# Performance work log

Hardware: AMD Instinct MI355X
Metric: run time of the kernel (lower is better)

Reference implementation:

```python
import jax, jax.numpy as jnp
import numpy as np

D_POINTS = 256
D_MODEL = 512
B, N = 8, 2048


def setup_inputs() -> dict:
    key = jax.random.key(0)
    ks = jax.random.split(key, 6)
    s_in = 1.0 / np.sqrt(D_POINTS)
    s_mid = 1.0 / np.sqrt(D_MODEL)
    return {
        "features": jax.random.normal(ks[0], (B, N, D_POINTS), dtype=jnp.float32),
        "Wq": jax.random.uniform(ks[1], (D_POINTS, D_MODEL), jnp.float32, -s_in, s_in),
        "Wk": jax.random.uniform(ks[2], (D_POINTS, D_MODEL), jnp.float32, -s_in, s_in),
        "Wv": jax.random.uniform(ks[3], (D_POINTS, D_MODEL), jnp.float32, -s_in, s_in),
        "W2": jax.random.uniform(ks[4], (D_MODEL, D_POINTS), jnp.float32, -s_mid, s_mid),
        "b2": jax.random.uniform(ks[5], (D_POINTS,), jnp.float32, -s_mid, s_mid),
    }


def reference(features, Wq, Wk, Wv, W2, b2):
    # features: [B, N, d_points]
    q = jnp.einsum("bnd,dm->bnm", features, Wq)  # [B, N, d_model]
    k = jnp.einsum("bnd,dm->bnm", features, Wk)
    v = jnp.einsum("bnd,dm->bnm", features, Wv)
    scale = 1.0 / np.sqrt(k.shape[-1]).astype(np.float32)
    attn = jax.nn.softmax(jnp.einsum("bnm,bkm->bnk", q, k) * scale, axis=-1)  # [B, N, N]
    res = jnp.einsum("bnk,bkm->bnm", attn, v)  # [B, N, d_model]
    res = jnp.einsum("bnm,md->bnd", res, W2) + b2  # fc2 -> [B, N, d_points]
    res = jax.nn.leaky_relu(res, negative_slope=0.2)
    return res + features
```

## Files before the change

### kernel.cpp

```cpp
#include <hip/hip_runtime.h>
#include <cstdint>

#define NBATCH 8
#define NSEQ   2048
#define NROWS  16384

typedef __attribute__((ext_vector_type(4))) float  f32x4;
typedef __attribute__((ext_vector_type(8))) short  short8;
typedef __attribute__((ext_vector_type(8))) __bf16 bf16x8;
typedef __attribute__((ext_vector_type(8))) _Float16 h8;

#define XB_OFF   0ul
#define WALL_OFF 8388608ul
#define Q_OFF    9175040ul
#define K_OFF    25952256ul
#define VT_OFF   42729472ul
#define W2T_OFF  59506688ul
#define S_OFF    59768832ul

#define SCALE_Q 0.063758746f

__device__ __forceinline__ unsigned short f2bf(float f) {
  unsigned u = __builtin_bit_cast(unsigned, f);
  return (unsigned short)((u + 0x7fffu + ((u >> 16) & 1u)) >> 16);
}

__device__ __forceinline__ f32x4 mfma16(short8 a, short8 b, f32x4 c) {
  return __builtin_amdgcn_mfma_f32_16x16x32_bf16(
      __builtin_bit_cast(bf16x8, a), __builtin_bit_cast(bf16x8, b), c, 0, 0, 0);
}

__device__ __forceinline__ void glds16(const void* g, void* l) {
  __builtin_amdgcn_global_load_lds(
      (const __attribute__((address_space(1))) void*)g,
      (__attribute__((address_space(3))) void*)l, 16, 0, 0);
}

#define BAR_LGKM()                                           \
  {                                                          \
    asm volatile("s_waitcnt lgkmcnt(0)" ::: "memory");       \
    __builtin_amdgcn_sched_barrier(0);                       \
    __builtin_amdgcn_s_barrier();                            \
    __builtin_amdgcn_sched_barrier(0);                       \
  }
#define BAR_ALL()                                                    \
  {                                                                  \
    asm volatile("s_waitcnt vmcnt(0) lgkmcnt(0)" ::: "memory");      \
    __builtin_amdgcn_sched_barrier(0);                               \
    __builtin_amdgcn_s_barrier();                                    \
    __builtin_amdgcn_sched_barrier(0);                               \
  }

__global__ __launch_bounds__(256, 4) void prep_kernel(
    const float* __restrict__ feat, const float* __restrict__ Wq,
    const float* __restrict__ Wk, const float* __restrict__ Wv,
    const float* __restrict__ W2, char* __restrict__ ws) {
  int tid = blockIdx.x * 256 + threadIdx.x;
  if (tid < 524288) {
    int r = tid >> 5, co = (tid & 31) * 8;
    const float* src = feat + (size_t)r * 256 + co;
    short8 v;
#pragma unroll
    for (int i = 0; i < 8; ++i) v[i] = (short)f2bf(src[i]);
    unsigned short* Xb = (unsigned short*)(ws + XB_OFF);
    *(short8*)(Xb + (size_t)r * 256 + (co ^ ((r & 7) << 3))) = v;
  } else if (tid < 917504) {
    int t2 = tid - 524288;
    int m = t2 >> 8, d = t2 & 255;
    int wsel = m >> 9, mm = m & 511;
    const float* W = (wsel == 0) ? Wq : ((wsel == 1) ? Wk : Wv);
    float v = W[(size_t)d * 512 + mm];
    if (wsel == 0) v *= SCALE_Q;
    unsigned short* Wall = (unsigned short*)(ws + WALL_OFF);
    Wall[(size_t)m * 256 + (d ^ ((m & 7) << 3))] = f2bf(v);
  } else {
    int t3 = tid - 917504;
    int d = t3 >> 9, c = t3 & 511;
    unsigned short* W2t = (unsigned short*)(ws + W2T_OFF);
    W2t[(size_t)d * 512 + c] = f2bf(W2[(size_t)c * 256 + d]);
  }
}

__global__ __launch_bounds__(256, 2) void proj_kernel(char* __restrict__ ws) {
  __shared__ char smem[65536];
  const int tid = threadIdx.x;
  const int l = tid & 63, w = tid >> 6;
  const int g = l >> 4, m16 = l & 15;
  const int orig = blockIdx.x;
  const int wgid = (orig & 7) * 192 + (orig >> 3);
  const int nt = wgid % 12, mtb = wgid / 12;
  const char* XbT = ws + XB_OFF + (size_t)mtb * 65536;
  const char* WallT = ws + WALL_OFF + (size_t)nt * 65536;

  auto stage = [&](int buf, int kt) {
#pragma unroll
    for (int j = 0; j < 4; ++j) {
      int idx = j * 256 + tid;
      int r = idx >> 3, p = idx & 7;
      glds16(XbT + r * 512 + kt * 128 + p * 16, smem + buf * 16384 + idx * 16);
      glds16(WallT + r * 512 + kt * 128 + p * 16,
             smem + 32768 + buf * 16384 + idx * 16);
    }
  };

  const int mr = (w >> 1) * 64, nr = (w & 1) * 64;
  const int fxor = (m16 & 7) << 4;
  const f32x4 fz = {0.f, 0.f, 0.f, 0.f};
  f32x4 acc[4][4];
#pragma unroll
  for (int i = 0; i < 4; ++i)
#pragma unroll
    for (int j = 0; j < 4; ++j) acc[i][j] = fz;

  stage(0, 0);
  BAR_ALL();
#pragma unroll 1
  for (int kt = 0; kt < 4; ++kt) {
    if (kt < 3) stage((kt + 1) & 1, kt + 1);
    const char* Ab = smem + (kt & 1) * 16384;
    const char* Bb = smem + 32768 + (kt & 1) * 16384;
#pragma unroll
    for (int ks = 0; ks < 2; ++ks) {
      int off = (16 * g + 64 * ks) ^ fxor;
      short8 af[4], bf[4];
#pragma unroll
      for (int i = 0; i < 4; ++i)
        af[i] = *(const short8*)(Ab + (mr + i * 16 + m16) * 128 + off);
#pragma unroll
      for (int i = 0; i < 4; ++i)
        bf[i] = *(const short8*)(Bb + (nr + i * 16 + m16) * 128 + off);
#pragma unroll
      for (int mi = 0; mi < 4; ++mi)
#pragma unroll
        for (int ni = 0; ni < 4; ++ni)
          acc[mi][ni] = mfma16(af[mi], bf[ni], acc[mi][ni]);
    }
    BAR_ALL();
  }

  const int colg = nt * 128 + nr;
  const int tcat = colg >> 9;
  const int cin_base = colg & 511;
  char* wbuf = smem + w * 2048;
  if (tcat < 2) {
    char* dst = ws + (tcat == 0 ? Q_OFF : K_OFF) +
                ((size_t)(mtb * 8 + (cin_base >> 6))) * 16384;
#pragma unroll
    for (int mi = 0; mi < 4; ++mi) {
#pragma unroll
      for (int ni = 0; ni < 4; ++ni)
#pragma unroll
        for (int j = 0; j < 4; ++j) {
          int r = g * 4 + j, c = ni * 16 + m16;
          *(unsigned short*)(wbuf + r * 128 + ((2 * c) ^ ((r & 7) << 4))) =
              f2bf(acc[mi][ni][j]);
        }
      asm volatile("s_waitcnt lgkmcnt(0)" ::: "memory");
      __builtin_amdgcn_sched_barrier(0);
#pragma unroll
      for (int s = 0; s < 2; ++s) {
        int cid = l + 64 * s;
        int r2 = cid >> 3, gi = cid & 7;
        short8 v = *(const short8*)(wbuf + r2 * 128 + gi * 16);
        int rt = mr + mi * 16 + r2;
        *(short8*)(dst + (size_t)rt * 128 + gi * 16) = v;
      }
    }
  } else {
    short8 grans[8];
#pragma unroll
    for (int mi = 0; mi < 4; ++mi) {
#pragma unroll
      for (int ni = 0; ni < 4; ++ni)
#pragma unroll
        for (int j = 0; j < 4; ++j) {
          int r = g * 4 + j, c = ni * 16 + m16;
          *(unsigned short*)(wbuf + r * 128 + ((2 * c) ^ ((r & 7) << 4))) =
              f2bf(acc[mi][ni][j]);
        }
      asm volatile("s_waitcnt lgkmcnt(0)" ::: "memory");
      __builtin_amdgcn_sched_barrier(0);
      unsigned short vals[16];
#pragma unroll
      for (int r2 = 0; r2 < 16; ++r2)
        vals[r2] = *(const unsigned short*)(wbuf + r2 * 128 +
                                            ((2 * l) ^ ((r2 & 7) << 4)));
      short8 v0, v1;
#pragma unroll
      for (int i2 = 0; i2 < 8; ++i2) {
        v0[i2] = (short)vals[i2];
        v1[i2] = (short)vals[8 + i2];
      }
      grans[2 * mi] = v0;
      grans[2 * mi + 1] = v1;
    }
    int cin = cin_base + l;
    int grow0 = mtb * 128 + mr;
    int bb = grow0 >> 11;
    int ktv = (grow0 & 2047) >> 6;
    char* vrow = ws + VT_OFF + (size_t)bb * 2097152 + (size_t)ktv * 65536 +
                 (size_t)cin * 128;
    const int fc = (cin & 7) << 4;
#pragma unroll
    for (int t = 0; t < 8; ++t)
      *(short8*)(vrow + ((t * 16) ^ fc)) = grans[t];
  }
}

__global__ __launch_bounds__(256, 2) void qk_kernel(
    const char* __restrict__ ws, char* __restrict__ Sb, int nb, int b0) {
  __shared__ char smem[65536];
  const int tid = threadIdx.x;
  const int bid = blockIdx.x;
  const int z = bid % nb, tile = bid / nb;
  const int mt = tile >> 4, ntq = tile & 15;
  const int b = b0 + z;
  const int l = tid & 63, w = tid >> 6;
  const int g = l >> 4, m16 = l & 15;
  const int fxor = (m16 & 7) << 4;
  const char* Qt = ws + Q_OFF + (size_t)(b * 16 + mt) * 131072;
  const char* Kt = ws + K_OFF + (size_t)(b * 16 + ntq) * 131072;

  auto stage = [&](int buf, int kt) {
#pragma unroll
    for (int j = 0; j < 4; ++j) {
      int idx = j * 256 + tid;
      glds16(Qt + (size_t)kt * 16384 + idx * 16, smem + buf * 16384 + idx * 16);
      glds16(Kt + (size_t)kt * 16384 + idx * 16,
             smem + 32768 + buf * 16384 + idx * 16);
    }
  };

  const int mr = (w >> 1) * 64, nr = (w & 1) * 64;
  const f32x4 fz = {0.f, 0.f, 0.f, 0.f};
  f32x4 acc[4][4];
#pragma unroll
  for (int i = 0; i < 4; ++i)
#pragma unroll
    for (int j = 0; j < 4; ++j) acc[i][j] = fz;

  stage(0, 0);
  BAR_ALL();
#pragma unroll 1
  for (int kt = 0; kt < 8; ++kt) {
    if (kt < 7) stage((kt + 1) & 1, kt + 1);
    const char* Ab = smem + (kt & 1) * 16384;
    const char* Bb = smem + 32768 + (kt & 1) * 16384;
#pragma unroll
    for (int ks = 0; ks < 2; ++ks) {
      int off = (16 * g + 64 * ks) ^ fxor;
      short8 af[4], bf[4];
#pragma unroll
      for (int i = 0; i < 4; ++i)
        af[i] = *(const short8*)(Ab + (mr + i * 16 + m16) * 128 + off);
#pragma unroll
      for (int i = 0; i < 4; ++i)
        bf[i] = *(const short8*)(Bb + (nr + i * 16 + m16) * 128 + off);
#pragma unroll
      for (int mi = 0; mi < 4; ++mi)
#pragma unroll
        for (int ni = 0; ni < 4; ++ni)
          acc[mi][ni] = mfma16(af[mi], bf[ni], acc[mi][ni]);
    }
    BAR_ALL();
  }

#pragma unroll
  for (int mi = 0; mi < 4; ++mi)
#pragma unroll
    for (int ni = 0; ni < 4; ++ni)
#pragma unroll
      for (int j = 0; j < 4; ++j) {
        int r = mr + mi * 16 + g * 4 + j, c = nr + ni * 16 + m16;
        *(unsigned short*)(smem + r * 272 + 2 * c) =
            __builtin_bit_cast(unsigned short, (_Float16)acc[mi][ni][j]);
      }
  BAR_LGKM();
  char* Sbt = Sb + (size_t)z * 8388608;
#pragma unroll
  for (int it = 0; it < 8; ++it) {
    int idx = it * 256 + tid;
    int r = idx >> 4, gi = idx & 15;
    int rg = mt * 2 + (r >> 6), ck = ntq * 2 + (gi >> 3);
    *(short8*)(Sbt + ((size_t)(rg * 32 + ck) * 64 + (r & 63)) * 128 +
               (gi & 7) * 16) = *(const short8*)(smem + r * 272 + gi * 16);
  }
}

__global__ __launch_bounds__(256, 4) void stats_kernel(char* __restrict__ Sb) {
  const int w = threadIdx.x >> 6, l = threadIdx.x & 63;
  const size_t row = (size_t)blockIdx.x * 4 + w;
  const int z = (int)(row >> 11), rloc = (int)(row & 2047);
  const int rg = rloc >> 6, r64 = rloc & 63;
  const int f = (rloc & 7) << 4;
  char* base = Sb + (size_t)z * 8388608 + (size_t)rg * 262144 +
               (size_t)r64 * 128;
  float sv[32];
#pragma unroll
  for (int i = 0; i < 4; ++i) {
    int idx = i * 64 + l;
    int ck = idx >> 3, gi = idx & 7;
    h8 hv = *(const h8*)(base + (size_t)ck * 8192 + gi * 16);
#pragma unroll
    for (int j = 0; j < 8; ++j) sv[i * 8 + j] = (float)hv[j];
  }
  float m = sv[0];
#pragma unroll
  for (int i = 1; i < 32; ++i) m = fmaxf(m, sv[i]);
  m = fmaxf(m, __shfl_xor(m, 1));
  m = fmaxf(m, __shfl_xor(m, 2));
  m = fmaxf(m, __shfl_xor(m, 4));
  m = fmaxf(m, __shfl_xor(m, 8));
  m = fmaxf(m, __shfl_xor(m, 16));
  m = fmaxf(m, __shfl_xor(m, 32));
  float sum = 0.f;
#pragma unroll
  for (int i = 0; i < 32; ++i) {
    float p = exp2f(sv[i] - m);
    sv[i] = p;
    sum += p;
  }
  sum += __shfl_xor(sum, 1);
  sum += __shfl_xor(sum, 2);
  sum += __shfl_xor(sum, 4);
  sum += __shfl_xor(sum, 8);
  sum += __shfl_xor(sum, 16);
  sum += __shfl_xor(sum, 32);
  const float rs = 1.0f / sum;
#pragma unroll
  for (int i = 0; i < 4; ++i) {
    int idx = i * 64 + l;
    int ck = idx >> 3, gi = idx & 7;
    short8 pk;
#pragma unroll
    for (int j = 0; j < 8; ++j) pk[j] = (short)f2bf(sv[i * 8 + j] * rs);
    *(short8*)(base + (size_t)ck * 8192 + ((gi * 16) ^ f)) = pk;
  }
}

__global__ __launch_bounds__(512, 2) void pv_kernel(
    const char* __restrict__ ws, const char* __restrict__ Sb,
    const float* __restrict__ feat, const float* __restrict__ b2,
    float* __restrict__ out, int nb, int b0) {
  __shared__ char smem[147456];
  const int tid = threadIdx.x;
  const int bid = blockIdx.x;
  const int z = bid % nb, mt64 = bid / nb;
  const int b = b0 + z;
  const int l = tid & 63, w = tid >> 6;
  const int g = l >> 4, m16 = l & 15;
  const int fxor = (m16 & 7) << 4;
  const char* Pr = Sb + (size_t)z * 8388608 + (size_t)mt64 * 262144;
  const char* Vt = ws + VT_OFF + (size_t)b * 2097152;

  auto stage = [&](int buf, int kt) {
    glds16(Pr + (size_t)kt * 8192 + tid * 16, smem + buf * 8192 + tid * 16);
#pragma unroll
    for (int j = 0; j < 8; ++j) {
      int idx = j * 512 + tid;
      glds16(Vt + (size_t)kt * 65536 + idx * 16,
             smem + 16384 + buf * 65536 + idx * 16);
    }
  };

  const f32x4 fz = {0.f, 0.f, 0.f, 0.f};
  f32x4 acc[4][4];
#pragma unroll
  for (int i = 0; i < 4; ++i)
#pragma unroll
    for (int j = 0; j < 4; ++j) acc[i][j] = fz;

  stage(0, 0);
  BAR_ALL();
#pragma unroll 1
  for (int kt = 0; kt < 32; ++kt) {
    if (kt < 31) stage((kt + 1) & 1, kt + 1);
    const char* Ab = smem + (kt & 1) * 8192;
    const char* Vb = smem + 16384 + (kt & 1) * 65536 + w * 8192;
#pragma unroll
    for (int ks = 0; ks < 2; ++ks) {
      int off = (16 * g + 64 * ks) ^ fxor;
      short8 af[4], vf[4];
#pragma unroll
      for (int i = 0; i < 4; ++i)
        af[i] = *(const short8*)(Ab + (i * 16 + m16) * 128 + off);
#pragma unroll
      for (int i = 0; i < 4; ++i)
        vf[i] = *(const short8*)(Vb + (i * 16 + m16) * 128 + off);
#pragma unroll
      for (int mi = 0; mi < 4; ++mi)
#pragma unroll
        for (int ni = 0; ni < 4; ++ni)
          acc[mi][ni] = mfma16(af[mi], vf[ni], acc[mi][ni]);
    }
    BAR_ALL();
  }

  char* Ob = smem + 16384;
#pragma unroll
  for (int mi = 0; mi < 4; ++mi)
#pragma unroll
    for (int ni = 0; ni < 4; ++ni)
#pragma unroll
      for (int j = 0; j < 4; ++j) {
        int r = mi * 16 + g * 4 + j;
        int c = w * 64 + ni * 16 + m16;
        *(unsigned short*)(Ob + r * 1024 + ((2 * c) ^ ((r & 7) << 4))) =
            f2bf(acc[mi][ni][j]);
      }
  BAR_LGKM();

  const char* W2g = ws + W2T_OFF;
  f32x4 y[4][2];
#pragma unroll
  for (int i = 0; i < 4; ++i) {
    y[i][0] = fz;
    y[i][1] = fz;
  }
#pragma unroll 1
  for (int ks = 0; ks < 16; ++ks) {
    int off = (ks * 64 + 16 * g);
    short8 aa[4], wb[2];
#pragma unroll
    for (int mi2 = 0; mi2 < 4; ++mi2) {
      int r = mi2 * 16 + m16;
      aa[mi2] = *(const short8*)(Ob + r * 1024 + (off ^ fxor));
    }
#pragma unroll
    for (int ni2 = 0; ni2 < 2; ++ni2) {
      int d = w * 32 + ni2 * 16 + m16;
      wb[ni2] = *(const short8*)(W2g + (size_t)d * 1024 + ks * 64 + g * 16);
    }
#pragma unroll
    for (int mi2 = 0; mi2 < 4; ++mi2)
#pragma unroll
      for (int ni2 = 0; ni2 < 2; ++ni2)
        y[mi2][ni2] = mfma16(aa[mi2], wb[ni2], y[mi2][ni2]);
  }
#pragma unroll
  for (int mi2 = 0; mi2 < 4; ++mi2)
#pragma unroll
    for (int ni2 = 0; ni2 < 2; ++ni2) {
      int d = w * 32 + ni2 * 16 + m16;
      float bias = b2[d];
#pragma unroll
      for (int j = 0; j < 4; ++j) {
        size_t gr = (size_t)b * 2048 + mt64 * 64 + mi2 * 16 + g * 4 + j;
        float v = y[mi2][ni2][j] + bias;
        v = v > 0.f ? v : 0.2f * v;
        out[gr * 256 + d] = v + feat[gr * 256 + d];
      }
    }
}

extern "C" void kernel_launch(void* const* d_in, const int* in_sizes, int n_in,
                              void* d_out, int out_size, void* d_ws, size_t ws_size,
                              hipStream_t stream) {
  const float* feat = (const float*)d_in[0];
  const float* Wq = (const float*)d_in[1];
  const float* Wk = (const float*)d_in[2];
  const float* Wv = (const float*)d_in[3];
  const float* W2 = (const float*)d_in[4];
  const float* b2 = (const float*)d_in[5];
  float* out = (float*)d_out;
  char* ws = (char*)d_ws;
  (void)in_sizes; (void)n_in; (void)out_size;

  prep_kernel<<<4096, 256, 0, stream>>>(feat, Wq, Wk, Wv, W2, ws);
  proj_kernel<<<1536, 256, 0, stream>>>(ws);

  const size_t per_batch = 8388608ul;
  int nb = 8;
  while (nb > 1 && S_OFF + (size_t)nb * per_batch > ws_size) nb >>= 1;
  char* Sb = ws + S_OFF;
  for (int b0 = 0; b0 < 8; b0 += nb) {
    qk_kernel<<<256 * nb, 256, 0, stream>>>(ws, Sb, nb, b0);
    stats_kernel<<<512 * nb, 256, 0, stream>>>(Sb);
    pv_kernel<<<32 * nb, 512, 0, stream>>>(ws, Sb, feat, b2, out, nb, b0);
  }
}
```

Measured before the change: 153.8 us.

## Use 3-stage half-K pipelines with partial vmcnt waits in QK and PV

The QK and PV GEMM main loops change from double-buffered 64-wide K tiles with full vmcnt(0) barriers to triple-buffered 32-wide K tiles. Each iteration waits with a partial vmcnt count, so two stages of global-to-LDS loads stay in flight while the MFMAs run. The V-transpose layout written by prep and the LDS swizzle (XOR over 4 granules) change to match the 64-byte rows, and the stats kernel swizzle is updated with them. Smaller LDS footprints allow higher occupancy hints. The cost is twice as many barriers per K, plus a risk of layout mismatch across kernels.

```diff
diff --git a/kernel.cpp b/kernel.cpp
--- a/kernel.cpp
+++ b/kernel.cpp
@@ -36,6 +36,12 @@
       (__attribute__((address_space(3))) void*)l, 16, 0, 0);
 }
 
+#define BAR_SYNC()                    \
+  {                                   \
+    __builtin_amdgcn_sched_barrier(0);\
+    __builtin_amdgcn_s_barrier();     \
+    __builtin_amdgcn_sched_barrier(0);\
+  }
 #define BAR_LGKM()                                           \
   {                                                          \
     asm volatile("s_waitcnt lgkmcnt(0)" ::: "memory");       \
@@ -152,7 +158,7 @@
 #pragma unroll
         for (int j = 0; j < 4; ++j) {
           int r = g * 4 + j, c = ni * 16 + m16;
-          *(unsigned short*)(wbuf + r * 128 + ((2 * c) ^ ((r & 7) << 4))) =
+          *(unsigned short*)(wbuf + r * 128 + ((2 * c) ^ ((r & 3) << 4))) =
               f2bf(acc[mi][ni][j]);
         }
       asm volatile("s_waitcnt lgkmcnt(0)" ::: "memory");
@@ -175,7 +181,7 @@
 #pragma unroll
         for (int j = 0; j < 4; ++j) {
           int r = g * 4 + j, c = ni * 16 + m16;
-          *(unsigned short*)(wbuf + r * 128 + ((2 * c) ^ ((r & 7) << 4))) =
+          *(unsigned short*)(wbuf + r * 128 + ((2 * c) ^ ((r & 3) << 4))) =
               f2bf(acc[mi][ni][j]);
         }
       asm volatile("s_waitcnt lgkmcnt(0)" ::: "memory");
@@ -184,7 +190,7 @@
 #pragma unroll
       for (int r2 = 0; r2 < 16; ++r2)
         vals[r2] = *(const unsigned short*)(wbuf + r2 * 128 +
-                                            ((2 * l) ^ ((r2 & 7) << 4)));
+                                            ((2 * l) ^ ((r2 & 3) << 4)));
       short8 v0, v1;
 #pragma unroll
       for (int i2 = 0; i2 < 8; ++i2) {
@@ -197,19 +203,22 @@
     int cin = cin_base + l;
     int grow0 = mtb * 128 + mr;
     int bb = grow0 >> 11;
-    int ktv = (grow0 & 2047) >> 6;
-    char* vrow = ws + VT_OFF + (size_t)bb * 2097152 + (size_t)ktv * 65536 +
-                 (size_t)cin * 128;
-    const int fc = (cin & 7) << 4;
-#pragma unroll
-    for (int t = 0; t < 8; ++t)
-      *(short8*)(vrow + ((t * 16) ^ fc)) = grans[t];
-  }
-}
-
-__global__ __launch_bounds__(256, 2) void qk_kernel(
+    int kt32 = (grow0 & 2047) >> 5;
+    char* vbase = ws + VT_OFF + (size_t)bb * 2097152 + (size_t)kt32 * 32768 +
+                  (size_t)cin * 64;
+    const int fc = (cin & 3) << 4;
+#pragma unroll
+    for (int t = 0; t < 4; ++t)
+      *(short8*)(vbase + ((t * 16) ^ fc)) = grans[t];
+#pragma unroll
+    for (int t = 0; t < 4; ++t)
+      *(short8*)(vbase + 32768 + ((t * 16) ^ fc)) = grans[4 + t];
+  }
+}
+
+__global__ __launch_bounds__(256, 3) void qk_kernel(
     const char* __restrict__ ws, char* __restrict__ Sb, int nb, int b0) {
-  __shared__ char smem[65536];
+  __shared__ char smem[49152];
   const int tid = threadIdx.x;
   const int bid = blockIdx.x;
   const int z = bid % nb, tile = bid / nb;
@@ -217,17 +226,20 @@
   const int b = b0 + z;
   const int l = tid & 63, w = tid >> 6;
   const int g = l >> 4, m16 = l & 15;
-  const int fxor = (m16 & 7) << 4;
+  const int afo = (16 * g) ^ ((m16 & 3) << 4);
   const char* Qt = ws + Q_OFF + (size_t)(b * 16 + mt) * 131072;
   const char* Kt = ws + K_OFF + (size_t)(b * 16 + ntq) * 131072;
 
-  auto stage = [&](int buf, int kt) {
-#pragma unroll
-    for (int j = 0; j < 4; ++j) {
+  auto stage = [&](int buf, int kt2) {
+    const char* qs = Qt + (size_t)(kt2 >> 1) * 16384 + (kt2 & 1) * 64;
+    const char* ks2 = Kt + (size_t)(kt2 >> 1) * 16384 + (kt2 & 1) * 64;
+    char* d = smem + buf * 16384;
+#pragma unroll
+    for (int j = 0; j < 2; ++j) {
       int idx = j * 256 + tid;
-      glds16(Qt + (size_t)kt * 16384 + idx * 16, smem + buf * 16384 + idx * 16);
-      glds16(Kt + (size_t)kt * 16384 + idx * 16,
-             smem + 32768 + buf * 16384 + idx * 16);
+      int r = idx >> 2, c4 = idx & 3;
+      glds16(qs + r * 128 + c4 * 16, d + idx * 16);
+      glds16(ks2 + r * 128 + c4 * 16, d + 8192 + idx * 16);
     }
   };
 
@@ -240,29 +252,36 @@
     for (int j = 0; j < 4; ++j) acc[i][j] = fz;
 
   stage(0, 0);
-  BAR_ALL();
+  stage(1, 1);
+  int cur = 0, pre = 2;
 #pragma unroll 1
-  for (int kt = 0; kt < 8; ++kt) {
-    if (kt < 7) stage((kt + 1) & 1, kt + 1);
-    const char* Ab = smem + (kt & 1) * 16384;
-    const char* Bb = smem + 32768 + (kt & 1) * 16384;
-#pragma unroll
-    for (int ks = 0; ks < 2; ++ks) {
-      int off = (16 * g + 64 * ks) ^ fxor;
-      short8 af[4], bf[4];
-#pragma unroll
-      for (int i = 0; i < 4; ++i)
-        af[i] = *(const short8*)(Ab + (mr + i * 16 + m16) * 128 + off);
-#pragma unroll
-      for (int i = 0; i < 4; ++i)
-        bf[i] = *(const short8*)(Bb + (nr + i * 16 + m16) * 128 + off);
-#pragma unroll
-      for (int mi = 0; mi < 4; ++mi)
-#pragma unroll
-        for (int ni = 0; ni < 4; ++ni)
-          acc[mi][ni] = mfma16(af[mi], bf[ni], acc[mi][ni]);
-    }
-    BAR_ALL();
+  for (int kt = 0; kt < 16; ++kt) {
+    if (kt < 14) {
+      stage(pre, kt + 2);
+      asm volatile("s_waitcnt vmcnt(8)" ::: "memory");
+    } else if (kt == 14) {
+      asm volatile("s_waitcnt vmcnt(4)" ::: "memory");
+    } else {
+      asm volatile("s_waitcnt vmcnt(0)" ::: "memory");
+    }
+    BAR_SYNC();
+    const char* Ab = smem + cur * 16384;
+    const char* Bb = Ab + 8192;
+    short8 af[4], bf[4];
+#pragma unroll
+    for (int i = 0; i < 4; ++i)
+      af[i] = *(const short8*)(Ab + (mr + i * 16 + m16) * 64 + afo);
+#pragma unroll
+    for (int i = 0; i < 4; ++i)
+      bf[i] = *(const short8*)(Bb + (nr + i * 16 + m16) * 64 + afo);
+#pragma unroll
+    for (int mi = 0; mi < 4; ++mi)
+#pragma unroll
+      for (int ni = 0; ni < 4; ++ni)
+        acc[mi][ni] = mfma16(af[mi], bf[ni], acc[mi][ni]);
+    BAR_LGKM();
+    cur = (cur == 2) ? 0 : cur + 1;
+    pre = (pre == 2) ? 0 : pre + 1;
   }
 
 #pragma unroll
@@ -287,12 +306,12 @@
   }
 }
 
-__global__ __launch_bounds__(256, 4) void stats_kernel(char* __restrict__ Sb) {
+__global__ __launch_bounds__(256, 6) void stats_kernel(char* __restrict__ Sb) {
   const int w = threadIdx.x >> 6, l = threadIdx.x & 63;
   const size_t row = (size_t)blockIdx.x * 4 + w;
   const int z = (int)(row >> 11), rloc = (int)(row & 2047);
   const int rg = rloc >> 6, r64 = rloc & 63;
-  const int f = (rloc & 7) << 4;
+  const int f = (rloc & 3) << 4;
   char* base = Sb + (size_t)z * 8388608 + (size_t)rg * 262144 +
                (size_t)r64 * 128;
   float sv[32];
@@ -342,24 +361,32 @@
     const char* __restrict__ ws, const char* __restrict__ Sb,
     const float* __restrict__ feat, const float* __restrict__ b2,
     float* __restrict__ out, int nb, int b0) {
-  __shared__ char smem[147456];
+  __shared__ char smem[114688];
   const int tid = threadIdx.x;
   const int bid = blockIdx.x;
   const int z = bid % nb, mt64 = bid / nb;
   const int b = b0 + z;
   const int l = tid & 63, w = tid >> 6;
   const int g = l >> 4, m16 = l & 15;
+  const int afo = (16 * g) ^ ((m16 & 3) << 4);
   const int fxor = (m16 & 7) << 4;
   const char* Pr = Sb + (size_t)z * 8388608 + (size_t)mt64 * 262144;
   const char* Vt = ws + VT_OFF + (size_t)b * 2097152;
 
-  auto stage = [&](int buf, int kt) {
-    glds16(Pr + (size_t)kt * 8192 + tid * 16, smem + buf * 8192 + tid * 16);
-#pragma unroll
-    for (int j = 0; j < 8; ++j) {
+  auto stage = [&](int buf, int kt2) {
+    {
+      int idx = (w & 3) * 64 + l;
+      int r64 = idx >> 2, c4 = idx & 3;
+      glds16(Pr + (size_t)(kt2 >> 1) * 8192 + r64 * 128 + (kt2 & 1) * 64 +
+                 c4 * 16,
+             smem + buf * 4096 + idx * 16);
+    }
+    const char* vsrc = Vt + (size_t)kt2 * 32768;
+    char* vdst = smem + 16384 + buf * 32768;
+#pragma unroll
+    for (int j = 0; j < 4; ++j) {
       int idx = j * 512 + tid;
-      glds16(Vt + (size_t)kt * 65536 + idx * 16,
-             smem + 16384 + buf * 65536 + idx * 16);
+      glds16(vsrc + idx * 16, vdst + idx * 16);
     }
   };
 
@@ -371,29 +398,36 @@
     for (int j = 0; j < 4; ++j) acc[i][j] = fz;
 
   stage(0, 0);
-  BAR_ALL();
+  stage(1, 1);
+  int cur = 0, pre = 2;
 #pragma unroll 1
-  for (int kt = 0; kt < 32; ++kt) {
-    if (kt < 31) stage((kt + 1) & 1, kt + 1);
-    const char* Ab = smem + (kt & 1) * 8192;
-    const char* Vb = smem + 16384 + (kt & 1) * 65536 + w * 8192;
-#pragma unroll
-    for (int ks = 0; ks < 2; ++ks) {
-      int off = (16 * g + 64 * ks) ^ fxor;
-      short8 af[4], vf[4];
-#pragma unroll
-      for (int i = 0; i < 4; ++i)
-        af[i] = *(const short8*)(Ab + (i * 16 + m16) * 128 + off);
-#pragma unroll
-      for (int i = 0; i < 4; ++i)
-        vf[i] = *(const short8*)(Vb + (i * 16 + m16) * 128 + off);
-#pragma unroll
-      for (int mi = 0; mi < 4; ++mi)
-#pragma unroll
-        for (int ni = 0; ni < 4; ++ni)
-          acc[mi][ni] = mfma16(af[mi], vf[ni], acc[mi][ni]);
-    }
-    BAR_ALL();
+  for (int kt = 0; kt < 64; ++kt) {
+    if (kt < 62) {
+      stage(pre, kt + 2);
+      asm volatile("s_waitcnt vmcnt(10)" ::: "memory");
+    } else if (kt == 62) {
+      asm volatile("s_waitcnt vmcnt(5)" ::: "memory");
+    } else {
+      asm volatile("s_waitcnt vmcnt(0)" ::: "memory");
+    }
+    BAR_SYNC();
+    const char* Ab = smem + cur * 4096;
+    const char* Vb = smem + 16384 + cur * 32768 + w * 4096;
+    short8 af[4], vf[4];
+#pragma unroll
+    for (int i = 0; i < 4; ++i)
+      af[i] = *(const short8*)(Ab + (i * 16 + m16) * 64 + afo);
+#pragma unroll
+    for (int i = 0; i < 4; ++i)
+      vf[i] = *(const short8*)(Vb + (i * 16 + m16) * 64 + afo);
+#pragma unroll
+    for (int mi = 0; mi < 4; ++mi)
+#pragma unroll
+      for (int ni = 0; ni < 4; ++ni)
+        acc[mi][ni] = mfma16(af[mi], vf[ni], acc[mi][ni]);
+    BAR_LGKM();
+    cur = (cur == 2) ? 0 : cur + 1;
+    pre = (pre == 2) ? 0 : pre + 1;
   }
 
   char* Ob = smem + 16384;
```

Measured after the change: 164.3 us. 6.8% more time.

## Load P fragments directly to registers in PV kernel, drop P LDS staging

Applied to the files above, without the earlier changes.

The PV kernel now loads the normalized probability tile straight from global memory into register fragments (double-buffered across two register sets) instead of staging it through LDS, so the LDS allocation shrinks and the main loop is unrolled by two. The stats kernel writes P unswizzled to match the new direct register loads, and its occupancy hint is raised. This removes LDS traffic and bank pressure for P but adds register pressure and exposes global-load latency inside the loop. The launch bound on the PV kernel is also relaxed.

```diff
diff --git a/kernel.cpp b/kernel.cpp
--- a/kernel.cpp
+++ b/kernel.cpp
@@ -155,8 +155,8 @@
           *(unsigned short*)(wbuf + r * 128 + ((2 * c) ^ ((r & 7) << 4))) =
               f2bf(acc[mi][ni][j]);
         }
-      asm volatile("s_waitcnt lgkmcnt(0)" ::: "memory");
-      __builtin_amdgcn_sched_barrier(0);
+    asm volatile("s_waitcnt lgkmcnt(0)" ::: "memory");
+    __builtin_amdgcn_sched_barrier(0);
 #pragma unroll
       for (int s = 0; s < 2; ++s) {
         int cid = l + 64 * s;
@@ -287,12 +287,11 @@
   }
 }
 
-__global__ __launch_bounds__(256, 4) void stats_kernel(char* __restrict__ Sb) {
+__global__ __launch_bounds__(256, 8) void stats_kernel(char* __restrict__ Sb) {
   const int w = threadIdx.x >> 6, l = threadIdx.x & 63;
   const size_t row = (size_t)blockIdx.x * 4 + w;
   const int z = (int)(row >> 11), rloc = (int)(row & 2047);
   const int rg = rloc >> 6, r64 = rloc & 63;
-  const int f = (rloc & 7) << 4;
   char* base = Sb + (size_t)z * 8388608 + (size_t)rg * 262144 +
                (size_t)r64 * 128;
   float sv[32];
@@ -334,15 +333,15 @@
     short8 pk;
 #pragma unroll
     for (int j = 0; j < 8; ++j) pk[j] = (short)f2bf(sv[i * 8 + j] * rs);
-    *(short8*)(base + (size_t)ck * 8192 + ((gi * 16) ^ f)) = pk;
-  }
-}
-
-__global__ __launch_bounds__(512, 2) void pv_kernel(
+    *(short8*)(base + (size_t)ck * 8192 + gi * 16) = pk;
+  }
+}
+
+__global__ __launch_bounds__(512) void pv_kernel(
     const char* __restrict__ ws, const char* __restrict__ Sb,
     const float* __restrict__ feat, const float* __restrict__ b2,
     float* __restrict__ out, int nb, int b0) {
-  __shared__ char smem[147456];
+  __shared__ char smem[131072];
   const int tid = threadIdx.x;
   const int bid = blockIdx.x;
   const int z = bid % nb, mt64 = bid / nb;
@@ -353,50 +352,68 @@
   const char* Pr = Sb + (size_t)z * 8388608 + (size_t)mt64 * 262144;
   const char* Vt = ws + VT_OFF + (size_t)b * 2097152;
 
-  auto stage = [&](int buf, int kt) {
-    glds16(Pr + (size_t)kt * 8192 + tid * 16, smem + buf * 8192 + tid * 16);
+  const f32x4 fz = {0.f, 0.f, 0.f, 0.f};
+  f32x4 acc[4][4];
+#pragma unroll
+  for (int i = 0; i < 4; ++i)
+#pragma unroll
+    for (int j = 0; j < 4; ++j) acc[i][j] = fz;
+
+  auto stageV = [&](int buf, int kt) {
 #pragma unroll
     for (int j = 0; j < 8; ++j) {
       int idx = j * 512 + tid;
       glds16(Vt + (size_t)kt * 65536 + idx * 16,
-             smem + 16384 + buf * 65536 + idx * 16);
+             smem + buf * 65536 + idx * 16);
     }
   };
-
-  const f32x4 fz = {0.f, 0.f, 0.f, 0.f};
-  f32x4 acc[4][4];
-#pragma unroll
-  for (int i = 0; i < 4; ++i)
-#pragma unroll
-    for (int j = 0; j < 4; ++j) acc[i][j] = fz;
-
-  stage(0, 0);
+  auto loadP = [&](short8(&pf)[8], int kt) {
+    const char* Pk = Pr + (size_t)kt * 8192 + m16 * 128 + g * 16;
+#pragma unroll
+    for (int mi = 0; mi < 4; ++mi)
+#pragma unroll
+      for (int ks = 0; ks < 2; ++ks)
+        pf[mi * 2 + ks] = *(const short8*)(Pk + mi * 2048 + ks * 64);
+  };
+  auto compute = [&](int buf, short8(&pf)[8]) {
+    const char* Vb = smem + buf * 65536 + w * 8192;
+#pragma unroll
+    for (int ks = 0; ks < 2; ++ks) {
+      int off = (16 * g + 64 * ks) ^ fxor;
+      short8 vf[4];
+#pragma unroll
+      for (int i = 0; i < 4; ++i)
+        vf[i] = *(const short8*)(Vb + (i * 16 + m16) * 128 + off);
+#pragma unroll
+      for (int mi = 0; mi < 4; ++mi)
+#pragma unroll
+        for (int ni = 0; ni < 4; ++ni)
+          acc[mi][ni] = mfma16(pf[mi * 2 + ks], vf[ni], acc[mi][ni]);
+    }
+  };
+
+  short8 pA[8], pB[8];
+  loadP(pA, 0);
+  stageV(0, 0);
   BAR_ALL();
 #pragma unroll 1
-  for (int kt = 0; kt < 32; ++kt) {
-    if (kt < 31) stage((kt + 1) & 1, kt + 1);
-    const char* Ab = smem + (kt & 1) * 8192;
-    const char* Vb = smem + 16384 + (kt & 1) * 65536 + w * 8192;
-#pragma unroll
-    for (int ks = 0; ks < 2; ++ks) {
-      int off = (16 * g + 64 * ks) ^ fxor;
-      short8 af[4], vf[4];
-#pragma unroll
-      for (int i = 0; i < 4; ++i)
-        af[i] = *(const short8*)(Ab + (i * 16 + m16) * 128 + off);
-#pragma unroll
-      for (int i = 0; i < 4; ++i)
-        vf[i] = *(const short8*)(Vb + (i * 16 + m16) * 128 + off);
-#pragma unroll
-      for (int mi = 0; mi < 4; ++mi)
-#pragma unroll
-        for (int ni = 0; ni < 4; ++ni)
-          acc[mi][ni] = mfma16(af[mi], vf[ni], acc[mi][ni]);
-    }
+  for (int kt2 = 0; kt2 < 16; ++kt2) {
+    const int kt = kt2 * 2;
+    if (kt + 1 < 32) {
+      loadP(pB, kt + 1);
+      stageV(1, kt + 1);
+    }
+    compute(0, pA);
     BAR_ALL();
-  }
-
-  char* Ob = smem + 16384;
+    if (kt + 2 < 32) {
+      loadP(pA, kt + 2);
+      stageV(0, kt + 2);
+    }
+    compute(1, pB);
+    BAR_ALL();
+  }
+
+  char* Ob = smem;
 #pragma unroll
   for (int mi = 0; mi < 4; ++mi)
 #pragma unroll
```

Result: slower. 204.9 us (+33.2%).
